# Optimization experiments

Measured on AMD Instinct MI355X. Metric: run time of the kernel, lower is better.

## Reference

```python
import jax, jax.numpy as jnp
import numpy as np

RANKS_HIGH = 15   # dt.RANKS.HIGH in the repo
SUITS_HIGH = 14   # padded so conv output last dim == 10 (Linear(10,32))
EPS = 1e-5


def _bn(x, g, b, axes):
    # Batch-norm over `axes` with channel dim = 1, training-mode batch stats.
    m = jnp.mean(x, axis=axes, keepdims=True)
    v = jnp.var(x, axis=axes, keepdims=True)
    xn = (x - m) * jax.lax.rsqrt(v + EPS)
    shp = [1] * x.ndim
    shp[1] = -1
    return xn * g.reshape(shp) + b.reshape(shp)


def setup_inputs() -> dict:
    key = jax.random.key(0)
    ks = jax.random.split(key, 16)
    M = 4096
    s = 0.05
    return {
        "x": jax.random.randint(ks[0], (M, 5, 2), 0, 4),  # (rank, suit) indices
        "conv_w": jax.random.normal(ks[1], (64, 5, 5, 5), jnp.float32) * s,
        "conv_b": jax.random.normal(ks[2], (64,), jnp.float32) * s,
        "bn0_g": jnp.ones((64,), jnp.float32),
        "bn0_b": jnp.zeros((64,), jnp.float32),
        "w_rank": jax.random.normal(ks[3], (32, 10), jnp.float32) * s,
        "b_rank": jax.random.normal(ks[4], (32,), jnp.float32) * s,
        "w_h1": jax.random.normal(ks[5], (32, 32), jnp.float32) * s,
        "b_h1": jax.random.normal(ks[6], (32,), jnp.float32) * s,
        "bn1_g": jnp.ones((64,), jnp.float32),
        "bn1_b": jnp.zeros((64,), jnp.float32),
        "w_h2": jax.random.normal(ks[7], (16, 32), jnp.float32) * s,
        "b_h2": jax.random.normal(ks[8], (16,), jnp.float32) * s,
        "bn2_g": jnp.ones((64,), jnp.float32),
        "bn2_b": jnp.zeros((64,), jnp.float32),
        "w_out": jax.random.normal(ks[9], (9, 11264), jnp.float32) * s,
        "b_out": jax.random.normal(ks[10], (9,), jnp.float32) * s,
    }


def reference(x, conv_w, conv_b, bn0_g, bn0_b, w_rank, b_rank, w_h1, b_h1,
              bn1_g, bn1_b, w_h2, b_h2, bn2_g, bn2_b, w_out, b_out):
    ranks = x[:, :, 0]
    suits = x[:, :, 1]
    # Vectorized replacement of the double Python-loop one-hot scatter:
    # three_d[j, i, ranks[j, i], suits[j, i]] = 1  ->  outer product of one-hots.
    three_d = (jax.nn.one_hot(ranks, RANKS_HIGH, dtype=jnp.float32)[..., :, None]
               * jax.nn.one_hot(suits, SUITS_HIGH, dtype=jnp.float32)[..., None, :])  # [M,5,15,14]
    r = jax.lax.conv_general_dilated(
        three_d, conv_w, window_strides=(1, 1), padding="VALID",
        dimension_numbers=("NCHW", "OIHW", "NCHW"))  # [M,64,11,10]
    r = r + conv_b[None, :, None, None]
    r = jax.nn.relu(_bn(r, bn0_g, bn0_b, (0, 2, 3)))
    r = jax.nn.relu(jnp.einsum("mchs,os->mcho", r, w_rank) + b_rank)      # [M,64,11,32]
    r = jnp.einsum("mchi,oi->mcho", r, w_h1) + b_h1                        # [M,64,11,32]
    r = jax.nn.relu(_bn(r, bn1_g, bn1_b, (0, 2, 3)))
    r = jnp.einsum("mchi,oi->mcho", r, w_h2) + b_h2                        # [M,64,11,16]
    r = jax.nn.relu(_bn(r, bn2_g, bn2_b, (0, 2, 3)))
    r = r.reshape(r.shape[0], -1)                                          # [M,11264]
    return r @ w_out.T + b_out                                             # [M,9]
```

## Files before the change

kernel.cpp:

```cpp
#include <hip/hip_runtime.h>
#include <hip/hip_bf16.h>

#define EPSV 1e-5f

typedef float vf2 __attribute__((ext_vector_type(2)));
typedef _Float16 h4f __attribute__((ext_vector_type(4)));

__device__ __forceinline__ vf2 pk_fma(vf2 a, vf2 b, vf2 c) {
  vf2 d;
  asm("v_pk_fma_f32 %0, %1, %2, %3" : "=v"(d) : "v"(a), "v"(b), "v"(c));
  return d;
}
__device__ __forceinline__ vf2 pk_mul(vf2 a, vf2 b) {
  vf2 d;
  asm("v_pk_mul_f32 %0, %1, %2" : "=v"(d) : "v"(a), "v"(b));
  return d;
}

#define WS_SUM0   0
#define WS_SSQ0   64
#define WS_SUM1   128
#define WS_SSQ1   192
#define WS_SUM2   256
#define WS_SSQ2   320
#define WS_AL0    384
#define WS_BE0    448
#define WS_ZBG    512
#define WS_T1BG   576
#define WS_AL1    2624
#define WS_BE1    2688
#define WS_T2BG   2752
#define WS_AL2    3776
#define WS_BE2    3840
#define WS_A2BG   3904
#define WS_OC     4928
#define WS_CU     4992
#define WS_CW     5120
#define WS_HIST   10304
#define WS_WSUM   13056
#define WS_T1     24576

#define CONV_LDS 5184
#define NHIST 2640

__device__ __forceinline__ void stage_conv(float* sW, const float* __restrict__ conv_w,
                                           int nthr) {
  for (int i = threadIdx.x; i < 8000; i += nthr) {
    int k = i / 125, rem = i - k * 125;
    int cc = rem / 25, r2 = rem - cc * 25;
    int di = r2 / 5, dj = r2 - di * 5;
    if (di < 4 && dj < 4) sW[k * 81 + cc * 16 + di * 4 + dj] = conv_w[i];
  }
  for (int k = threadIdx.x; k < 64; k += nthr) sW[k * 81 + 80] = 0.f;
}

__device__ __forceinline__ void stage_conv_fast(float* sW, const float* __restrict__ cw) {
  const float4* src = (const float4*)cw;
  float4* dst = (float4*)sW;
  for (int i = threadIdx.x; i < CONV_LDS / 4; i += 256) dst[i] = src[i];
}

__device__ __forceinline__ int conv_idx(int di, int dj, int cc) {
  int idx = cc * 16 + di * 4 + dj;
  return ((di | dj) >= 0) ? idx : 80;
}

__global__ __launch_bounds__(256) void k_prep3(
    const int* __restrict__ x, const float* __restrict__ conv_w,
    const float* __restrict__ w_out, float* __restrict__ ws, int M) {
  __shared__ float h[NHIST];
  const int b = blockIdx.x;
  const int tid = threadIdx.x;
  if (b < 8) {
    float* cw = ws + WS_CW;
    const int gid = b * 256 + tid;
    for (int i = gid; i < 8000; i += 8 * 256) {
      int k = i / 125, rem = i - k * 125;
      int cc = rem / 25, r2 = rem - cc * 25;
      int di = r2 / 5, dj = r2 - di * 5;
      if (di < 4 && dj < 4) cw[k * 81 + cc * 16 + di * 4 + dj] = conv_w[i];
    }
    for (int k = gid; k < 64; k += 8 * 256) cw[k * 81 + 80] = 0.f;
  } else if (b < 44) {
    const int gid = (b - 8) * 256 + tid;
    if (gid < 9216) {
      int j = gid / 1024, kp = gid - j * 1024;
      int k = kp >> 4, p = kp & 15;
      float s = 0.f;
#pragma unroll
      for (int yy = 4; yy < 11; ++yy)
        s += w_out[j * 11264 + k * 176 + yy * 16 + p];
      ws[WS_WSUM + gid] = s;
    }
  } else {
    for (int i = tid; i < NHIST; i += 256) h[i] = 0.f;
    __syncthreads();
    for (int m = (b - 44) * 256 + tid; m < M; m += 16 * 256) {
      int v[5];
      const int2* xp = (const int2*)(x + m * 10);
#pragma unroll
      for (int cc = 0; cc < 5; ++cc) {
        int2 t = xp[cc];
        v[cc] = (t.x << 2) | t.y;
      }
#pragma unroll
      for (int cc = 0; cc < 5; ++cc) atomicAdd(&h[cc * 16 + v[cc]], 1.f);
      int pr = 0;
#pragma unroll
      for (int a = 0; a < 5; ++a)
#pragma unroll
        for (int bb = a + 1; bb < 5; ++bb) {
          atomicAdd(&h[80 + pr * 256 + v[a] * 16 + v[bb]], 1.f);
          ++pr;
        }
    }
    __syncthreads();
    for (int i = tid; i < NHIST; i += 256)
      if (h[i] != 0.f) atomicAdd(&ws[WS_HIST + i], h[i]);
  }
}

__global__ __launch_bounds__(256) void k_stats0h(
    const float* __restrict__ conv_b, float* __restrict__ ws, int M) {
  __shared__ float sWk[81];
  __shared__ float sH[NHIST];
  const int tid = threadIdx.x;
  const int k = blockIdx.x;
  if (tid < 81) sWk[tid] = ws[WS_CW + k * 81 + tid];
  for (int i = tid; i < NHIST; i += 256) sH[i] = ws[WS_HIST + i];
  __syncthreads();
  const float cb = conv_b[k];
  float L = 0.f, Q = 0.f, P = 0.f;
  for (int it = tid; it < 1280; it += 256) {
    int pos = it / 80, rem = it - pos * 80;
    int cc = rem >> 4, v = rem & 15;
    int y = pos >> 2, xx = pos & 3;
    float w = sWk[conv_idx((v >> 2) - y, (v & 3) - xx, cc)];
    float n = sH[cc * 16 + v];
    L += n * w;
    Q += n * w * w;
  }
  if (tid < 160) {
    int pos = tid / 10, pr = tid - pos * 10;
    int y = pos >> 2, xx = pos & 3;
    int a, b;
    if (pr < 4)      { a = 0; b = pr + 1; }
    else if (pr < 7) { a = 1; b = pr - 2; }
    else if (pr < 9) { a = 2; b = pr - 4; }
    else             { a = 3; b = 4; }
    const float* Hp = sH + 80 + pr * 256;
    for (int v1 = 0; v1 < 16; ++v1) {
      float w1 = sWk[conv_idx((v1 >> 2) - y, (v1 & 3) - xx, a)];
      float acc = 0.f;
#pragma unroll
      for (int v2 = 0; v2 < 16; ++v2) {
        float w2 = sWk[conv_idx((v2 >> 2) - y, (v2 & 3) - xx, b)];
        acc += Hp[v1 * 16 + v2] * w2;
      }
      P += w1 * acc;
    }
  }
  atomicAdd(&ws[WS_SUM0 + k], L);
  atomicAdd(&ws[WS_SSQ0 + k], Q + 2.f * cb * L + 2.f * P);
  if (tid == 0) {
    const float a16 = 16.f * (float)M;
    atomicAdd(&ws[WS_SUM0 + k], a16 * cb);
    atomicAdd(&ws[WS_SSQ0 + k], a16 * cb * cb);
  }
}

__global__ __launch_bounds__(256) void k_t1(
    const int* __restrict__ x, const float* __restrict__ conv_b,
    const float* __restrict__ g0, const float* __restrict__ b0,
    const float* __restrict__ w_rank, const float* __restrict__ b_rank,
    const float* __restrict__ w_h1, const float* __restrict__ b_h1,
    float* __restrict__ ws, float* __restrict__ t1, int M) {
  __shared__ float sW[CONV_LDS];
  __shared__ float sCU[32];
  stage_conv_fast(sW, ws + WS_CW);
  if (threadIdx.x < 32) {
    float cuv = 0.f;
    for (int s2 = 4; s2 < 10; ++s2) cuv += w_rank[threadIdx.x * 10 + s2];
    sCU[threadIdx.x] = cuv;
  }
  __syncthreads();
  const int tid = threadIdx.x;
  const int y = tid & 3, k = tid >> 2;
  const float cb = conv_b[k];
  const float n0 = 110.f * (float)M;
  const float S0  = ws[WS_SUM0 + k] + 94.f * (float)M * cb;
  const float SS0 = ws[WS_SSQ0 + k] + 94.f * (float)M * cb * cb;
  const float mu0 = S0 / n0;
  const float var0 = SS0 / n0 - mu0 * mu0;
  const float al = rsqrtf(var0 + EPSV) * g0[k];
  const float be = b0[k] - mu0 * al;
  const float zbg = fmaxf(cb * al + be, 0.f);
  const float* Wk = &sW[k * 81];
  const vf2* wrp = (const vf2*)w_rank;
  const vf2* w1p = (const vf2*)w_h1;
  h4f* t1h = (h4f*)t1;
  float sAcc = 0.f, ssAcc = 0.f;
  const int NP = (M + 1) >> 1;
  for (int mp = blockIdx.x; mp < NP; mp += gridDim.x) {
    const int mA = mp * 2, mB = mA + 1;
    const bool hasB = (mB < M);
    const int mBs = hasB ? mB : mA;
    int rA[5], cA[5], rB[5], cBx[5];
    const int2* xpA = (const int2*)(x + mA * 10);
    const int2* xpB = (const int2*)(x + mBs * 10);
#pragma unroll
    for (int cc = 0; cc < 5; ++cc) {
      int2 tA = xpA[cc]; rA[cc] = tA.x; cA[cc] = tA.y;
      int2 tB = xpB[cc]; rB[cc] = tB.x; cBx[cc] = tB.y;
    }
    float a0A[4], a0B[4];
#pragma unroll
    for (int xx = 0; xx < 4; ++xx) {
      float vA = cb, vB = cb;
#pragma unroll
      for (int cc = 0; cc < 5; ++cc) {
        vA += Wk[conv_idx(rA[cc] - y, cA[cc] - xx, cc)];
        vB += Wk[conv_idx(rB[cc] - y, cBx[cc] - xx, cc)];
      }
      a0A[xx] = fmaxf(al * vA + be, 0.f);
      a0B[xx] = fmaxf(al * vB + be, 0.f);
    }
    vf2 aAp[2], aBp[2];
    aAp[0].x = a0A[0]; aAp[0].y = a0A[1];
    aAp[1].x = a0A[2]; aAp[1].y = a0A[3];
    aBp[0].x = a0B[0]; aBp[0].y = a0B[1];
    aBp[1].x = a0B[2]; aBp[1].y = a0B[3];
    __builtin_amdgcn_sched_barrier(0);
    vf2 r1A[16], r1B[16];
#pragma unroll
    for (int o2 = 0; o2 < 16; ++o2) {
      const int oa = 2 * o2, ob = oa + 1;
      vf2 w0 = wrp[oa * 5], w1 = wrp[oa * 5 + 1];
      vf2 w2 = wrp[ob * 5], w3 = wrp[ob * 5 + 1];
      const float basea = b_rank[oa] + zbg * sCU[oa];
      const float baseb = b_rank[ob] + zbg * sCU[ob];
      vf2 accAa = pk_mul(aAp[0], w0); accAa = pk_fma(aAp[1], w1, accAa);
      vf2 accAb = pk_mul(aAp[0], w2); accAb = pk_fma(aAp[1], w3, accAb);
      vf2 accBa = pk_mul(aBp[0], w0); accBa = pk_fma(aBp[1], w1, accBa);
      vf2 accBb = pk_mul(aBp[0], w2); accBb = pk_fma(aBp[1], w3, accBb);
      vf2 ra, rb;
      ra.x = fmaxf(basea + accAa.x + accAa.y, 0.f);
      ra.y = fmaxf(baseb + accAb.x + accAb.y, 0.f);
      rb.x = fmaxf(basea + accBa.x + accBa.y, 0.f);
      rb.y = fmaxf(baseb + accBb.x + accBb.y, 0.f);
      r1A[o2] = ra;
      r1B[o2] = rb;
    }
    __builtin_amdgcn_sched_barrier(0);
    float sBm = 0.f, ssBm = 0.f;
#pragma unroll
    for (int chv = 0; chv < 8; ++chv) {
      float accA[4], accB[4];
#pragma unroll
      for (int u = 0; u < 4; ++u) {
        const int o = chv * 4 + u;
        vf2 a2A = {0.f, 0.f}, a2B = {0.f, 0.f};
#pragma unroll
        for (int i = 0; i < 16; ++i) {
          vf2 w = w1p[o * 16 + i];
          a2A = pk_fma(r1A[i], w, a2A);
          a2B = pk_fma(r1B[i], w, a2B);
        }
        const float bb = b_h1[o];
        float aA = bb + a2A.x + a2A.y;
        float aB = bb + a2B.x + a2B.y;
        accA[u] = aA; accB[u] = aB;
        sAcc += aA; ssAcc += aA * aA;
        sBm += aB;  ssBm += aB * aB;
      }
      h4f stA;
      stA[0] = (_Float16)accA[0]; stA[1] = (_Float16)accA[1];
      stA[2] = (_Float16)accA[2]; stA[3] = (_Float16)accA[3];
      t1h[((size_t)mA * 8 + chv) * 256 + tid] = stA;
      if (hasB) {
        h4f stB;
        stB[0] = (_Float16)accB[0]; stB[1] = (_Float16)accB[1];
        stB[2] = (_Float16)accB[2]; stB[3] = (_Float16)accB[3];
        t1h[((size_t)mB * 8 + chv) * 256 + tid] = stB;
      }
      __builtin_amdgcn_sched_barrier(0);
    }
    if (hasB) { sAcc += sBm; ssAcc += ssBm; }
  }
  sAcc  += __shfl_xor(sAcc, 1);  sAcc  += __shfl_xor(sAcc, 2);
  ssAcc += __shfl_xor(ssAcc, 1); ssAcc += __shfl_xor(ssAcc, 2);
  if (y == 0) {
    atomicAdd(&ws[WS_SUM1 + k], sAcc);
    atomicAdd(&ws[WS_SSQ1 + k], ssAcc);
  }
}

__global__ __launch_bounds__(256) void k_mid(
    const float* __restrict__ conv_b, const float* __restrict__ g0,
    const float* __restrict__ b0, const float* __restrict__ w_rank,
    const float* __restrict__ b_rank, const float* __restrict__ w_h1,
    const float* __restrict__ b_h1, const float* __restrict__ g1,
    const float* __restrict__ b1, const float* __restrict__ w_h2,
    const float* __restrict__ b_h2, float* __restrict__ ws, int M) {
  __shared__ float sWr[320];
  __shared__ float sWh1[32 * 33];
  __shared__ float sWh2[16 * 33];
  __shared__ float sS[32], sZ[64];
  __shared__ float sR1[64 * 33];
  __shared__ float sT1b[64 * 33];
  const int tid = threadIdx.x;
  for (int i = tid; i < 320; i += 256) sWr[i] = w_rank[i];
  for (int i = tid; i < 1024; i += 256) sWh1[(i >> 5) * 33 + (i & 31)] = w_h1[i];
  for (int i = tid; i < 512; i += 256) sWh2[(i >> 5) * 33 + (i & 31)] = w_h2[i];
  if (tid < 64) {
    const float cb = conv_b[tid];
    const float n0 = 110.f * (float)M;
    const float S0  = ws[WS_SUM0 + tid] + 94.f * (float)M * cb;
    const float SS0 = ws[WS_SSQ0 + tid] + 94.f * (float)M * cb * cb;
    const float mu0 = S0 / n0;
    const float var0 = SS0 / n0 - mu0 * mu0;
    const float al = rsqrtf(var0 + EPSV) * g0[tid];
    const float be = b0[tid] - mu0 * al;
    sZ[tid] = fmaxf(cb * al + be, 0.f);
  }
  __syncthreads();
  if (tid < 32) {
    float s = 0.f;
    for (int s2 = 0; s2 < 10; ++s2) s += sWr[tid * 10 + s2];
    sS[tid] = s;
  }
  __syncthreads();
  const int k = tid >> 2, q = tid & 3;
  const float zbg = sZ[k];
#pragma unroll
  for (int u = 0; u < 8; ++u) {
    const int o = q * 8 + u;
    sR1[k * 33 + o] = fmaxf(zbg * sS[o] + b_rank[o], 0.f);
  }
  __syncthreads();
  float sb = 0.f, ssb = 0.f;
#pragma unroll
  for (int u = 0; u < 8; ++u) {
    const int o = q * 8 + u;
    float acc = b_h1[o];
#pragma unroll
    for (int i = 0; i < 32; ++i) acc += sR1[k * 33 + i] * sWh1[o * 33 + i];
    sT1b[k * 33 + o] = acc;
    sb += acc;
    ssb += acc * acc;
  }
  sb  += __shfl_xor(sb, 1);  sb  += __shfl_xor(sb, 2);
  ssb += __shfl_xor(ssb, 1); ssb += __shfl_xor(ssb, 2);
  const float n1 = (float)M * 11.f * 32.f;
  const float S1  = ws[WS_SUM1 + k] + 7.f * (float)M * sb;
  const float SS1 = ws[WS_SSQ1 + k] + 7.f * (float)M * ssb;
  const float mu1 = S1 / n1;
  const float var1 = SS1 / n1 - mu1 * mu1;
  const float al1 = rsqrtf(var1 + EPSV) * g1[k];
  const float be1 = b1[k] - mu1 * al1;
  if (q == 0) {
    ws[WS_AL1 + k] = al1;
    ws[WS_BE1 + k] = be1;
  }
  __syncthreads();
#pragma unroll
  for (int u = 0; u < 8; ++u) {
    const int o = q * 8 + u;
    sR1[k * 33 + o] = fmaxf(al1 * sT1b[k * 33 + o] + be1, 0.f);
  }
  __syncthreads();
  float sb2 = 0.f, ssb2 = 0.f;
#pragma unroll
  for (int v = 0; v < 4; ++v) {
    const int p = q * 4 + v;
    float acc = b_h2[p];
#pragma unroll
    for (int o = 0; o < 32; ++o) acc += sR1[k * 33 + o] * sWh2[p * 33 + o];
    ws[WS_T2BG + k * 16 + p] = acc;
    sb2 += acc;
    ssb2 += acc * acc;
  }
  sb2  += __shfl_xor(sb2, 1);  sb2  += __shfl_xor(sb2, 2);
  ssb2 += __shfl_xor(ssb2, 1); ssb2 += __shfl_xor(ssb2, 2);
  if (q == 0) {
    ws[WS_SUM2 + k] = 7.f * (float)M * sb2;
    ws[WS_SSQ2 + k] = 7.f * (float)M * ssb2;
  }
}

__global__ __launch_bounds__(256) void k_t2(
    const float* __restrict__ w_h2, const float* __restrict__ b_h2,
    float* __restrict__ ws, float* __restrict__ t1, int M) {
  const int tid = threadIdx.x;
  const int y = tid & 3, k = tid >> 2;
  const float al1 = ws[WS_AL1 + k], be1 = ws[WS_BE1 + k];
  const vf2* w2p = (const vf2*)w_h2;
  h4f* t1h = (h4f*)t1;
  float sAcc = 0.f, ssAcc = 0.f;
  const int NP = (M + 1) >> 1;
  for (int mp = blockIdx.x; mp < NP; mp += gridDim.x) {
    const int mA = mp * 2, mB = mA + 1;
    const bool hasB = (mB < M);
    const int mBs = hasB ? mB : mA;
    vf2 a1A[16], a1B[16];
#pragma unroll
    for (int chv = 0; chv < 8; ++chv) {
      h4f vA = t1h[((size_t)mA * 8 + chv) * 256 + tid];
      h4f vB = t1h[((size_t)mBs * 8 + chv) * 256 + tid];
      vf2 pA0, pA1, pB0, pB1;
      pA0.x = fmaxf(al1 * (float)vA[0] + be1, 0.f);
      pA0.y = fmaxf(al1 * (float)vA[1] + be1, 0.f);
      pA1.x = fmaxf(al1 * (float)vA[2] + be1, 0.f);
      pA1.y = fmaxf(al1 * (float)vA[3] + be1, 0.f);
      pB0.x = fmaxf(al1 * (float)vB[0] + be1, 0.f);
      pB0.y = fmaxf(al1 * (float)vB[1] + be1, 0.f);
      pB1.x = fmaxf(al1 * (float)vB[2] + be1, 0.f);
      pB1.y = fmaxf(al1 * (float)vB[3] + be1, 0.f);
      a1A[chv * 2] = pA0; a1A[chv * 2 + 1] = pA1;
      a1B[chv * 2] = pB0; a1B[chv * 2 + 1] = pB1;
    }
    __builtin_amdgcn_sched_barrier(0);
    float sBm = 0.f, ssBm = 0.f;
#pragma unroll
    for (int pv = 0; pv < 4; ++pv) {
      float accA[4], accB[4];
#pragma unroll
      for (int u = 0; u < 4; ++u) {
        const int p = pv * 4 + u;
        vf2 a2A = {0.f, 0.f}, a2B = {0.f, 0.f};
#pragma unroll
        for (int i = 0; i < 16; ++i) {
          vf2 w = w2p[p * 16 + i];
          a2A = pk_fma(a1A[i], w, a2A);
          a2B = pk_fma(a1B[i], w, a2B);
        }
        const float bb = b_h2[p];
        float aA = bb + a2A.x + a2A.y;
        float aB = bb + a2B.x + a2B.y;
        accA[u] = aA; accB[u] = aB;
        sAcc += aA; ssAcc += aA * aA;
        sBm += aB;  ssBm += aB * aB;
      }
      h4f stA;
      stA[0] = (_Float16)accA[0]; stA[1] = (_Float16)accA[1];
      stA[2] = (_Float16)accA[2]; stA[3] = (_Float16)accA[3];
      t1h[((size_t)mA * 8 + pv) * 256 + tid] = stA;
      if (hasB) {
        h4f stB;
        stB[0] = (_Float16)accB[0]; stB[1] = (_Float16)accB[1];
        stB[2] = (_Float16)accB[2]; stB[3] = (_Float16)accB[3];
        t1h[((size_t)mB * 8 + pv) * 256 + tid] = stB;
      }
      __builtin_amdgcn_sched_barrier(0);
    }
    if (hasB) { sAcc += sBm; ssAcc += ssBm; }
  }
  sAcc  += __shfl_xor(sAcc, 1);  sAcc  += __shfl_xor(sAcc, 2);
  ssAcc += __shfl_xor(ssAcc, 1); ssAcc += __shfl_xor(ssAcc, 2);
  if (y == 0) {
    atomicAdd(&ws[WS_SUM2 + k], sAcc);
    atomicAdd(&ws[WS_SSQ2 + k], ssAcc);
  }
}

__global__ __launch_bounds__(256) void k_fin2p(
    const float* __restrict__ g2, const float* __restrict__ b2,
    const float* __restrict__ b_out, float* __restrict__ ws, int M) {
  __shared__ float sT2b[1024];
  __shared__ float sWs[9216];
  __shared__ float sAl2[64], sBe2[64];
  __shared__ float red[64 * 9];
  const int tid = threadIdx.x;
  for (int i = tid; i < 1024; i += 256) sT2b[i] = ws[WS_T2BG + i];
  for (int i = tid; i < 9216; i += 256) sWs[i] = ws[WS_WSUM + i];
  if (tid < 64) {
    const int k = tid;
    const float n2 = (float)M * 11.f * 16.f;
    const float S = ws[WS_SUM2 + k], SS = ws[WS_SSQ2 + k];
    const float mu = S / n2;
    const float var = SS / n2 - mu * mu;
    const float al = rsqrtf(var + EPSV) * g2[k];
    const float be = b2[k] - mu * al;
    sAl2[k] = al; sBe2[k] = be;
    ws[WS_AL2 + k] = al;
    ws[WS_BE2 + k] = be;
  }
  __syncthreads();
  for (int u = tid; u < 576; u += 256) {
    const int k = u / 9, j = u - k * 9;
    const float al = sAl2[k], be = sBe2[k];
    float acc = 0.f;
#pragma unroll
    for (int p = 0; p < 16; ++p)
      acc += fmaxf(al * sT2b[k * 16 + p] + be, 0.f) * sWs[j * 1024 + k * 16 + p];
    red[k * 9 + j] = acc;
  }
  __syncthreads();
  if (tid < 9) {
    float acc = b_out[tid];
    for (int t = 0; t < 64; ++t) acc += red[t * 9 + tid];
    ws[WS_OC + tid] = acc;
  }
}

__global__ __launch_bounds__(256) void k_out(
    const float* __restrict__ w_out, const float* __restrict__ ws,
    const float* __restrict__ t1, float* __restrict__ out, int M) {
  __shared__ float sOC[9];
  __shared__ float sRedA[4][9], sRedB[4][9];
  if (threadIdx.x < 9) sOC[threadIdx.x] = ws[WS_OC + threadIdx.x];
  __syncthreads();
  const int tid = threadIdx.x;
  const int lane = tid & 63, wv = tid >> 6;
  const int y = tid & 3, k = tid >> 2;
  const float al2 = ws[WS_AL2 + k], be2 = ws[WS_BE2 + k];
  const float4* wo = (const float4*)(w_out + k * 176 + y * 16);
  const h4f* t2h = (const h4f*)t1;
  const int NP = (M + 1) >> 1;
  bool first = true;
  for (int mp = blockIdx.x; mp < NP; mp += gridDim.x) {
    if (!first) __syncthreads();
    first = false;
    const int mA = mp * 2, mB = mA + 1;
    const bool hasB = (mB < M);
    const int mBs = hasB ? mB : mA;
    vf2 a2A[8], a2B[8];
#pragma unroll
    for (int iv = 0; iv < 4; ++iv) {
      h4f vA = t2h[((size_t)mA * 8 + iv) * 256 + tid];
      h4f vB = t2h[((size_t)mBs * 8 + iv) * 256 + tid];
      vf2 pA0, pA1, pB0, pB1;
      pA0.x = fmaxf(al2 * (float)vA[0] + be2, 0.f);
      pA0.y = fmaxf(al2 * (float)vA[1] + be2, 0.f);
      pA1.x = fmaxf(al2 * (float)vA[2] + be2, 0.f);
      pA1.y = fmaxf(al2 * (float)vA[3] + be2, 0.f);
      pB0.x = fmaxf(al2 * (float)vB[0] + be2, 0.f);
      pB0.y = fmaxf(al2 * (float)vB[1] + be2, 0.f);
      pB1.x = fmaxf(al2 * (float)vB[2] + be2, 0.f);
      pB1.y = fmaxf(al2 * (float)vB[3] + be2, 0.f);
      a2A[iv * 2] = pA0; a2A[iv * 2 + 1] = pA1;
      a2B[iv * 2] = pB0; a2B[iv * 2 + 1] = pB1;
    }
    float poA[9], poB[9];
#pragma unroll
    for (int j = 0; j < 9; ++j) {
      float4 w0 = wo[j * 2816 + 0], w1 = wo[j * 2816 + 1];
      float4 w2 = wo[j * 2816 + 2], w3 = wo[j * 2816 + 3];
      vf2 aA = {0.f, 0.f}, aB = {0.f, 0.f};
      vf2 t;
      t.x = w0.x; t.y = w0.y; aA = pk_fma(a2A[0], t, aA); aB = pk_fma(a2B[0], t, aB);
      t.x = w0.z; t.y = w0.w; aA = pk_fma(a2A[1], t, aA); aB = pk_fma(a2B[1], t, aB);
      t.x = w1.x; t.y = w1.y; aA = pk_fma(a2A[2], t, aA); aB = pk_fma(a2B[2], t, aB);
      t.x = w1.z; t.y = w1.w; aA = pk_fma(a2A[3], t, aA); aB = pk_fma(a2B[3], t, aB);
      t.x = w2.x; t.y = w2.y; aA = pk_fma(a2A[4], t, aA); aB = pk_fma(a2B[4], t, aB);
      t.x = w2.z; t.y = w2.w; aA = pk_fma(a2A[5], t, aA); aB = pk_fma(a2B[5], t, aB);
      t.x = w3.x; t.y = w3.y; aA = pk_fma(a2A[6], t, aA); aB = pk_fma(a2B[6], t, aB);
      t.x = w3.z; t.y = w3.w; aA = pk_fma(a2A[7], t, aA); aB = pk_fma(a2B[7], t, aB);
      poA[j] = aA.x + aA.y;
      poB[j] = aB.x + aB.y;
    }
#pragma unroll
    for (int j = 0; j < 9; ++j) {
      float vA = poA[j], vB = poB[j];
      vA += __shfl_xor(vA, 1);  vB += __shfl_xor(vB, 1);
      vA += __shfl_xor(vA, 2);  vB += __shfl_xor(vB, 2);
      vA += __shfl_xor(vA, 4);  vB += __shfl_xor(vB, 4);
      vA += __shfl_xor(vA, 8);  vB += __shfl_xor(vB, 8);
      vA += __shfl_xor(vA, 16); vB += __shfl_xor(vB, 16);
      vA += __shfl_xor(vA, 32); vB += __shfl_xor(vB, 32);
      poA[j] = vA; poB[j] = vB;
    }
    if (lane == 0) {
#pragma unroll
      for (int j = 0; j < 9; ++j) { sRedA[wv][j] = poA[j]; sRedB[wv][j] = poB[j]; }
    }
    __syncthreads();
    if (tid < 9) {
      float acc = sOC[tid];
#pragma unroll
      for (int w2i = 0; w2i < 4; ++w2i) acc += sRedA[w2i][tid];
      out[mA * 9 + tid] = acc;
    } else if (tid >= 64 && tid < 73 && hasB) {
      const int j = tid - 64;
      float acc = sOC[j];
#pragma unroll
      for (int w2i = 0; w2i < 4; ++w2i) acc += sRedB[w2i][j];
      out[mB * 9 + j] = acc;
    }
  }
}

__global__ __launch_bounds__(64) void k_fin0(
    const float* __restrict__ conv_b, const float* __restrict__ g0,
    const float* __restrict__ b0, const float* __restrict__ w_rank,
    const float* __restrict__ b_rank, const float* __restrict__ w_h1,
    const float* __restrict__ b_h1, float* __restrict__ ws, int M) {
  __shared__ float sS[32];
  const int t = threadIdx.x;
  if (t < 32) {
    float su = 0.f;
    for (int s2 = 0; s2 < 10; ++s2) su += w_rank[t * 10 + s2];
    sS[t] = su;
    float cu = 0.f;
    for (int s2 = 4; s2 < 10; ++s2) cu += w_rank[t * 10 + s2];
    ws[WS_CU + t] = cu;
  }
  __syncthreads();
  const int k = t;
  const float n0 = 110.f * (float)M;
  const float cb = conv_b[k];
  const float S  = ws[WS_SUM0 + k] + 94.f * (float)M * cb;
  const float SS = ws[WS_SSQ0 + k] + 94.f * (float)M * cb * cb;
  const float mu = S / n0;
  const float var = SS / n0 - mu * mu;
  const float rstd = rsqrtf(var + EPSV);
  const float al = rstd * g0[k];
  const float be = b0[k] - mu * al;
  ws[WS_AL0 + k] = al;
  ws[WS_BE0 + k] = be;
  const float zbg = fmaxf(cb * al + be, 0.f);
  ws[WS_ZBG + k] = zbg;
  float r1bg[32];
#pragma unroll
  for (int o = 0; o < 32; ++o) r1bg[o] = fmaxf(zbg * sS[o] + b_rank[o], 0.f);
  float sb = 0.f, ssb = 0.f;
  for (int o = 0; o < 32; ++o) {
    float acc = b_h1[o];
#pragma unroll
    for (int i = 0; i < 32; ++i) acc += r1bg[i] * w_h1[o * 32 + i];
    ws[WS_T1BG + k * 32 + o] = acc;
    sb += acc;
    ssb += acc * acc;
  }
  ws[WS_SUM1 + k] = 7.f * (float)M * sb;
  ws[WS_SSQ1 + k] = 7.f * (float)M * ssb;
}

__global__ __launch_bounds__(64) void k_fin1(
    const float* __restrict__ g1, const float* __restrict__ b1,
    const float* __restrict__ w_h2, const float* __restrict__ b_h2,
    float* __restrict__ ws, int M) {
  const int k = threadIdx.x;
  const float n1 = (float)M * 11.f * 32.f;
  const float S = ws[WS_SUM1 + k], SS = ws[WS_SSQ1 + k];
  const float mu = S / n1;
  const float var = SS / n1 - mu * mu;
  const float rstd = rsqrtf(var + EPSV);
  const float al = rstd * g1[k];
  const float be = b1[k] - mu * al;
  ws[WS_AL1 + k] = al;
  ws[WS_BE1 + k] = be;
  float a1bg[32];
#pragma unroll
  for (int o = 0; o < 32; ++o)
    a1bg[o] = fmaxf(al * ws[WS_T1BG + k * 32 + o] + be, 0.f);
  float sb = 0.f, ssb = 0.f;
  for (int p = 0; p < 16; ++p) {
    float acc = b_h2[p];
#pragma unroll
    for (int o = 0; o < 32; ++o) acc += a1bg[o] * w_h2[p * 32 + o];
    ws[WS_T2BG + k * 16 + p] = acc;
    sb += acc;
    ssb += acc * acc;
  }
  ws[WS_SUM2 + k] = 7.f * (float)M * sb;
  ws[WS_SSQ2 + k] = 7.f * (float)M * ssb;
}

__global__ __launch_bounds__(256) void k_stats0(
    const int* __restrict__ x, const float* __restrict__ conv_w,
    const float* __restrict__ conv_b, float* __restrict__ ws, int M) {
  __shared__ float sW[CONV_LDS];
  stage_conv(sW, conv_w, 256);
  __syncthreads();
  const int tid = threadIdx.x;
  const int mg = tid & 3;
  const int k  = tid >> 2;
  const float cb = conv_b[k];
  const float* Wk = &sW[k * 81];
  float s = 0.f, ss = 0.f;
  for (int m = blockIdx.x * 4 + mg; m < M; m += gridDim.x * 4) {
    int r[5], c[5];
    const int2* xp = (const int2*)(x + m * 10);
#pragma unroll
    for (int cc = 0; cc < 5; ++cc) { int2 t = xp[cc]; r[cc] = t.x; c[cc] = t.y; }
#pragma unroll
    for (int y = 0; y < 4; ++y) {
#pragma unroll
      for (int xx = 0; xx < 4; ++xx) {
        float v = cb;
#pragma unroll
        for (int cc = 0; cc < 5; ++cc)
          v += Wk[conv_idx(r[cc] - y, c[cc] - xx, cc)];
        s += v;
        ss += v * v;
      }
      __builtin_amdgcn_sched_barrier(0);
    }
  }
  s  += __shfl_xor(s, 1);  s  += __shfl_xor(s, 2);
  ss += __shfl_xor(ss, 1); ss += __shfl_xor(ss, 2);
  if (mg == 0) {
    atomicAdd(&ws[WS_SUM0 + k], s);
    atomicAdd(&ws[WS_SSQ0 + k], ss);
  }
}

__global__ __launch_bounds__(256) void k_stats1(
    const int* __restrict__ x, const float* __restrict__ conv_w,
    const float* __restrict__ conv_b, const float* __restrict__ w_rank,
    const float* __restrict__ b_rank, const float* __restrict__ w_h1,
    const float* __restrict__ b_h1, float* __restrict__ ws, int M) {
  __shared__ float sW[CONV_LDS];
  stage_conv(sW, conv_w, 256);
  __syncthreads();
  const int tid = threadIdx.x;
  const int y = tid & 3, k = tid >> 2;
  const float cb = conv_b[k];
  const float al = ws[WS_AL0 + k], be = ws[WS_BE0 + k], zbg = ws[WS_ZBG + k];
  const float* Wk = &sW[k * 81];
  const float* cu = ws + WS_CU;
  float sAcc = 0.f, ssAcc = 0.f;
  for (int m = blockIdx.x; m < M; m += gridDim.x) {
    int r[5], c[5];
    const int2* xp = (const int2*)(x + m * 10);
#pragma unroll
    for (int cc = 0; cc < 5; ++cc) { int2 t = xp[cc]; r[cc] = t.x; c[cc] = t.y; }
    float a0[4];
#pragma unroll
    for (int xx = 0; xx < 4; ++xx) {
      float v = cb;
#pragma unroll
      for (int cc = 0; cc < 5; ++cc)
        v += Wk[conv_idx(r[cc] - y, c[cc] - xx, cc)];
      a0[xx] = fmaxf(al * v + be, 0.f);
    }
    __builtin_amdgcn_sched_barrier(0);
    float r1[32];
#pragma unroll
    for (int o = 0; o < 32; ++o) {
// ... 135 lines not shown
      for (int yy = 4; yy < 11; ++yy)
        wsum += w_out[j * 11264 + k * 176 + yy * 16 + p];
      acc += a2bg[p] * wsum;
    }
    red[k * 9 + j] = acc;
  }
  __syncthreads();
  if (k < 9) {
    float acc = b_out[k];
    for (int t = 0; t < 64; ++t) acc += red[t * 9 + k];
    ws[WS_OC + k] = acc;
  }
}

__global__ __launch_bounds__(256) void k_final(
    const int* __restrict__ x, const float* __restrict__ conv_w,
    const float* __restrict__ conv_b, const float* __restrict__ w_rank,
    const float* __restrict__ b_rank, const float* __restrict__ w_h1,
    const float* __restrict__ b_h1, const float* __restrict__ w_h2,
    const float* __restrict__ b_h2, const float* __restrict__ w_out,
    const float* __restrict__ ws, float* __restrict__ out, int M) {
  __shared__ float sW[CONV_LDS];
  __shared__ float sOC[9];
  __shared__ float sRed[4][9];
  stage_conv(sW, conv_w, 256);
  if (threadIdx.x < 9) sOC[threadIdx.x] = ws[WS_OC + threadIdx.x];
  __syncthreads();
  const int tid = threadIdx.x;
  const int lane = tid & 63, wv = tid >> 6;
  const int y = tid & 3, k = tid >> 2;
  const float cb = conv_b[k];
  const float al = ws[WS_AL0 + k], be = ws[WS_BE0 + k], zbg = ws[WS_ZBG + k];
  const float al1 = ws[WS_AL1 + k], be1 = ws[WS_BE1 + k];
  const float al2 = ws[WS_AL2 + k], be2 = ws[WS_BE2 + k];
  const float* Wk = &sW[k * 81];
  const float* cu = ws + WS_CU;
  const float4* wo = (const float4*)(w_out + k * 176 + y * 16);
  bool first = true;
  for (int m = blockIdx.x; m < M; m += gridDim.x) {
    if (!first) __syncthreads();
    first = false;
    int r[5], c[5];
    const int2* xp = (const int2*)(x + m * 10);
#pragma unroll
    for (int cc = 0; cc < 5; ++cc) { int2 t = xp[cc]; r[cc] = t.x; c[cc] = t.y; }
    float a0[4];
#pragma unroll
    for (int xx = 0; xx < 4; ++xx) {
      float v = cb;
#pragma unroll
      for (int cc = 0; cc < 5; ++cc)
        v += Wk[conv_idx(r[cc] - y, c[cc] - xx, cc)];
      a0[xx] = fmaxf(al * v + be, 0.f);
    }
    __builtin_amdgcn_sched_barrier(0);
    float r1[32];
#pragma unroll
    for (int o = 0; o < 32; ++o) {
      float acc = b_rank[o] + zbg * cu[o];
#pragma unroll
      for (int xx = 0; xx < 4; ++xx) acc += a0[xx] * w_rank[o * 10 + xx];
      r1[o] = fmaxf(acc, 0.f);
    }
    __builtin_amdgcn_sched_barrier(0);
    float t2[16];
#pragma unroll
    for (int p = 0; p < 16; ++p) t2[p] = b_h2[p];
#pragma unroll
    for (int ch = 0; ch < 4; ++ch) {
      float a1c[8];
#pragma unroll
      for (int u = 0; u < 8; ++u) {
        const int o = ch * 8 + u;
        float acc = b_h1[o];
#pragma unroll
        for (int i = 0; i < 32; ++i) acc += r1[i] * w_h1[o * 32 + i];
        a1c[u] = fmaxf(al1 * acc + be1, 0.f);
      }
      __builtin_amdgcn_sched_barrier(0);
#pragma unroll
      for (int p = 0; p < 16; ++p) {
        float acc = t2[p];
#pragma unroll
        for (int u = 0; u < 8; ++u) acc += a1c[u] * w_h2[p * 32 + ch * 8 + u];
        t2[p] = acc;
      }
      __builtin_amdgcn_sched_barrier(0);
    }
    float a2[16];
#pragma unroll
    for (int p = 0; p < 16; ++p) a2[p] = fmaxf(al2 * t2[p] + be2, 0.f);
    float po[9];
#pragma unroll
    for (int j = 0; j < 9; ++j) {
      float4 w0 = wo[j * 2816 + 0], w1 = wo[j * 2816 + 1];
      float4 w2 = wo[j * 2816 + 2], w3 = wo[j * 2816 + 3];
      po[j] = a2[0] * w0.x + a2[1] * w0.y + a2[2] * w0.z + a2[3] * w0.w
            + a2[4] * w1.x + a2[5] * w1.y + a2[6] * w1.z + a2[7] * w1.w
            + a2[8] * w2.x + a2[9] * w2.y + a2[10] * w2.z + a2[11] * w2.w
            + a2[12] * w3.x + a2[13] * w3.y + a2[14] * w3.z + a2[15] * w3.w;
    }
#pragma unroll
    for (int j = 0; j < 9; ++j) {
      float v = po[j];
      v += __shfl_xor(v, 1);
      v += __shfl_xor(v, 2);
      v += __shfl_xor(v, 4);
      v += __shfl_xor(v, 8);
      v += __shfl_xor(v, 16);
      v += __shfl_xor(v, 32);
      po[j] = v;
    }
    if (lane == 0) {
#pragma unroll
      for (int j = 0; j < 9; ++j) sRed[wv][j] = po[j];
    }
    __syncthreads();
    if (tid < 9) {
      float acc = sOC[tid];
#pragma unroll
      for (int w2i = 0; w2i < 4; ++w2i) acc += sRed[w2i][tid];
      out[m * 9 + tid] = acc;
    }
  }
}

extern "C" void kernel_launch(void* const* d_in, const int* in_sizes, int n_in,
                              void* d_out, int out_size, void* d_ws, size_t ws_size,
                              hipStream_t stream) {
  const int*   x      = (const int*)d_in[0];
  const float* conv_w = (const float*)d_in[1];
  const float* conv_b = (const float*)d_in[2];
  const float* bn0_g  = (const float*)d_in[3];
  const float* bn0_b  = (const float*)d_in[4];
  const float* w_rank = (const float*)d_in[5];
  const float* b_rank = (const float*)d_in[6];
  const float* w_h1   = (const float*)d_in[7];
  const float* b_h1   = (const float*)d_in[8];
  const float* bn1_g  = (const float*)d_in[9];
  const float* bn1_b  = (const float*)d_in[10];
  const float* w_h2   = (const float*)d_in[11];
  const float* b_h2   = (const float*)d_in[12];
  const float* bn2_g  = (const float*)d_in[13];
  const float* bn2_b  = (const float*)d_in[14];
  const float* w_out  = (const float*)d_in[15];
  const float* b_out  = (const float*)d_in[16];
  float* out = (float*)d_out;
  float* ws  = (float*)d_ws;
  const int M = in_sizes[0] / 10;
  const size_t need = ((size_t)WS_T1 + (size_t)M * 4096) * sizeof(float);
  const int NP = (M + 1) >> 1;
  const int gridp = NP < 2048 ? NP : 2048;

  hipMemsetAsync(ws, 0, 384 * sizeof(float), stream);

  if (ws_size >= need) {
    float* t1 = ws + WS_T1;
    hipMemsetAsync(ws + WS_HIST, 0, NHIST * sizeof(float), stream);
    k_prep3<<<60, 256, 0, stream>>>(x, conv_w, w_out, ws, M);
    k_stats0h<<<64, 256, 0, stream>>>(conv_b, ws, M);
    k_t1<<<gridp, 256, 0, stream>>>(x, conv_b, bn0_g, bn0_b, w_rank, b_rank,
                                    w_h1, b_h1, ws, t1, M);
    k_mid<<<1, 256, 0, stream>>>(conv_b, bn0_g, bn0_b, w_rank, b_rank, w_h1, b_h1,
                                 bn1_g, bn1_b, w_h2, b_h2, ws, M);
    k_t2<<<gridp, 256, 0, stream>>>(w_h2, b_h2, ws, t1, M);
    k_fin2p<<<1, 256, 0, stream>>>(bn2_g, bn2_b, b_out, ws, M);
    k_out<<<gridp, 256, 0, stream>>>(w_out, ws, t1, out, M);
  } else {
    k_stats0<<<512, 256, 0, stream>>>(x, conv_w, conv_b, ws, M);
    k_fin0<<<1, 64, 0, stream>>>(conv_b, bn0_g, bn0_b, w_rank, b_rank, w_h1, b_h1, ws, M);
    k_stats1<<<1024, 256, 0, stream>>>(x, conv_w, conv_b, w_rank, b_rank, w_h1, b_h1,
                                       ws, M);
    k_fin1<<<1, 64, 0, stream>>>(bn1_g, bn1_b, w_h2, b_h2, ws, M);
    k_stats2<<<1024, 256, 0, stream>>>(x, conv_w, conv_b, w_rank, b_rank, w_h1, b_h1,
                                       w_h2, b_h2, ws, M);
    k_fin2<<<1, 64, 0, stream>>>(bn2_g, bn2_b, w_out, b_out, ws, M);
    k_final<<<1024, 256, 0, stream>>>(x, conv_w, conv_b, w_rank, b_rank, w_h1, b_h1,
                                      w_h2, b_h2, w_out, ws, out, M);
  }
}
```

Before: 303.2 us.

## Drop memsets and k_mid launch; per-slice histograms and fold mid-stats into consumers

Removes the two hipMemsetAsync calls by writing per-slice histograms and having k_stats0h write, rather than atomically add, the stats and zero the later accumulators. The single-block k_mid kernel is removed: its BN0/BN1 background computations are recomputed redundantly in every k_t2 block and in k_fin2p, which now also derives the BN2 background stats. k_out replaces its shuffle-based output reduction with an LDS transpose and a two-level sum. Together these cut kernel launches and serialized tiny kernels, at the cost of redundant per-block recomputation and more LDS use.

```diff
diff --git a/kernel.cpp b/kernel.cpp
--- a/kernel.cpp
+++ b/kernel.cpp
@@ -36,9 +36,9 @@
 #define WS_OC     4928
 #define WS_CU     4992
 #define WS_CW     5120
-#define WS_HIST   10304
-#define WS_WSUM   13056
-#define WS_T1     24576
+#define WS_WSUM   10304
+#define WS_HSL    19584
+#define WS_T1     65536
 
 #define CONV_LDS 5184
 #define NHIST 2640
@@ -93,9 +93,10 @@
       ws[WS_WSUM + gid] = s;
     }
   } else {
+    const int slice = b - 44;
     for (int i = tid; i < NHIST; i += 256) h[i] = 0.f;
     __syncthreads();
-    for (int m = (b - 44) * 256 + tid; m < M; m += 16 * 256) {
+    for (int m = slice * 256 + tid; m < M; m += 16 * 256) {
       int v[5];
       const int2* xp = (const int2*)(x + m * 10);
 #pragma unroll
@@ -116,7 +117,7 @@
     }
     __syncthreads();
     for (int i = tid; i < NHIST; i += 256)
-      if (h[i] != 0.f) atomicAdd(&ws[WS_HIST + i], h[i]);
+      ws[WS_HSL + slice * NHIST + i] = h[i];
   }
 }
 
@@ -124,10 +125,16 @@
     const float* __restrict__ conv_b, float* __restrict__ ws, int M) {
   __shared__ float sWk[81];
   __shared__ float sH[NHIST];
+  __shared__ float sRed[8];
   const int tid = threadIdx.x;
   const int k = blockIdx.x;
   if (tid < 81) sWk[tid] = ws[WS_CW + k * 81 + tid];
-  for (int i = tid; i < NHIST; i += 256) sH[i] = ws[WS_HIST + i];
+  for (int i = tid; i < NHIST; i += 256) {
+    float s = 0.f;
+#pragma unroll
+    for (int sl = 0; sl < 16; ++sl) s += ws[WS_HSL + sl * NHIST + i];
+    sH[i] = s;
+  }
   __syncthreads();
   const float cb = conv_b[k];
   float L = 0.f, Q = 0.f, P = 0.f;
@@ -160,12 +167,26 @@
       P += w1 * acc;
     }
   }
-  atomicAdd(&ws[WS_SUM0 + k], L);
-  atomicAdd(&ws[WS_SSQ0 + k], Q + 2.f * cb * L + 2.f * P);
+  float A = L, B = Q + 2.f * cb * L + 2.f * P;
+  A += __shfl_xor(A, 1);  B += __shfl_xor(B, 1);
+  A += __shfl_xor(A, 2);  B += __shfl_xor(B, 2);
+  A += __shfl_xor(A, 4);  B += __shfl_xor(B, 4);
+  A += __shfl_xor(A, 8);  B += __shfl_xor(B, 8);
+  A += __shfl_xor(A, 16); B += __shfl_xor(B, 16);
+  A += __shfl_xor(A, 32); B += __shfl_xor(B, 32);
+  const int lane = tid & 63, wv = tid >> 6;
+  if (lane == 0) { sRed[wv * 2] = A; sRed[wv * 2 + 1] = B; }
+  __syncthreads();
   if (tid == 0) {
+    float At = sRed[0] + sRed[2] + sRed[4] + sRed[6];
+    float Bt = sRed[1] + sRed[3] + sRed[5] + sRed[7];
     const float a16 = 16.f * (float)M;
-    atomicAdd(&ws[WS_SUM0 + k], a16 * cb);
-    atomicAdd(&ws[WS_SSQ0 + k], a16 * cb * cb);
+    ws[WS_SUM0 + k] = At + a16 * cb;
+    ws[WS_SSQ0 + k] = Bt + a16 * cb * cb;
+    ws[WS_SUM1 + k] = 0.f;
+    ws[WS_SSQ1 + k] = 0.f;
+    ws[WS_SUM2 + k] = 0.f;
+    ws[WS_SSQ2 + k] = 0.f;
   }
 }
 
@@ -295,105 +316,55 @@
   }
 }
 
-__global__ __launch_bounds__(256) void k_mid(
+__global__ __launch_bounds__(256) void k_t2(
     const float* __restrict__ conv_b, const float* __restrict__ g0,
     const float* __restrict__ b0, const float* __restrict__ w_rank,
     const float* __restrict__ b_rank, const float* __restrict__ w_h1,
     const float* __restrict__ b_h1, const float* __restrict__ g1,
     const float* __restrict__ b1, const float* __restrict__ w_h2,
-    const float* __restrict__ b_h2, float* __restrict__ ws, int M) {
-  __shared__ float sWr[320];
-  __shared__ float sWh1[32 * 33];
-  __shared__ float sWh2[16 * 33];
-  __shared__ float sS[32], sZ[64];
-  __shared__ float sR1[64 * 33];
-  __shared__ float sT1b[64 * 33];
+    const float* __restrict__ b_h2, float* __restrict__ ws,
+    float* __restrict__ t1, int M) {
+  __shared__ float sS[32];
+  __shared__ float sWh1[1024];
   const int tid = threadIdx.x;
-  for (int i = tid; i < 320; i += 256) sWr[i] = w_rank[i];
-  for (int i = tid; i < 1024; i += 256) sWh1[(i >> 5) * 33 + (i & 31)] = w_h1[i];
-  for (int i = tid; i < 512; i += 256) sWh2[(i >> 5) * 33 + (i & 31)] = w_h2[i];
-  if (tid < 64) {
-    const float cb = conv_b[tid];
-    const float n0 = 110.f * (float)M;
-    const float S0  = ws[WS_SUM0 + tid] + 94.f * (float)M * cb;
-    const float SS0 = ws[WS_SSQ0 + tid] + 94.f * (float)M * cb * cb;
-    const float mu0 = S0 / n0;
-    const float var0 = SS0 / n0 - mu0 * mu0;
-    const float al = rsqrtf(var0 + EPSV) * g0[tid];
-    const float be = b0[tid] - mu0 * al;
-    sZ[tid] = fmaxf(cb * al + be, 0.f);
-  }
-  __syncthreads();
+  for (int i = tid; i < 1024; i += 256) sWh1[i] = w_h1[i];
   if (tid < 32) {
     float s = 0.f;
-    for (int s2 = 0; s2 < 10; ++s2) s += sWr[tid * 10 + s2];
+    for (int s2 = 0; s2 < 10; ++s2) s += w_rank[tid * 10 + s2];
     sS[tid] = s;
   }
   __syncthreads();
-  const int k = tid >> 2, q = tid & 3;
-  const float zbg = sZ[k];
+  const int y = tid & 3, k = tid >> 2;
+  const float fM = (float)M;
+  const float cb = conv_b[k];
+  const float n0 = 110.f * fM;
+  const float S0  = ws[WS_SUM0 + k] + 94.f * fM * cb;
+  const float SS0 = ws[WS_SSQ0 + k] + 94.f * fM * cb * cb;
+  const float mu0 = S0 / n0;
+  const float al0 = rsqrtf(SS0 / n0 - mu0 * mu0 + EPSV) * g0[k];
+  const float be0 = b0[k] - mu0 * al0;
+  const float zbg = fmaxf(cb * al0 + be0, 0.f);
+  float r1bg[32];
+#pragma unroll
+  for (int o = 0; o < 32; ++o) r1bg[o] = fmaxf(zbg * sS[o] + b_rank[o], 0.f);
+  float sb = 0.f, ssb = 0.f;
 #pragma unroll
   for (int u = 0; u < 8; ++u) {
-    const int o = q * 8 + u;
-    sR1[k * 33 + o] = fmaxf(zbg * sS[o] + b_rank[o], 0.f);
-  }
-  __syncthreads();
-  float sb = 0.f, ssb = 0.f;
-#pragma unroll
-  for (int u = 0; u < 8; ++u) {
-    const int o = q * 8 + u;
-    float acc = b_h1[o];
-#pragma unroll
-    for (int i = 0; i < 32; ++i) acc += sR1[k * 33 + i] * sWh1[o * 33 + i];
-    sT1b[k * 33 + o] = acc;
-    sb += acc;
-    ssb += acc * acc;
+    const int o = y * 8 + u;
+    float a = b_h1[o];
+#pragma unroll
+    for (int i = 0; i < 32; ++i) a += r1bg[i] * sWh1[o * 32 + i];
+    sb += a;
+    ssb += a * a;
   }
   sb  += __shfl_xor(sb, 1);  sb  += __shfl_xor(sb, 2);
   ssb += __shfl_xor(ssb, 1); ssb += __shfl_xor(ssb, 2);
-  const float n1 = (float)M * 11.f * 32.f;
-  const float S1  = ws[WS_SUM1 + k] + 7.f * (float)M * sb;
-  const float SS1 = ws[WS_SSQ1 + k] + 7.f * (float)M * ssb;
+  const float n1 = fM * 11.f * 32.f;
+  const float S1  = ws[WS_SUM1 + k] + 7.f * fM * sb;
+  const float SS1 = ws[WS_SSQ1 + k] + 7.f * fM * ssb;
   const float mu1 = S1 / n1;
-  const float var1 = SS1 / n1 - mu1 * mu1;
-  const float al1 = rsqrtf(var1 + EPSV) * g1[k];
+  const float al1 = rsqrtf(SS1 / n1 - mu1 * mu1 + EPSV) * g1[k];
   const float be1 = b1[k] - mu1 * al1;
-  if (q == 0) {
-    ws[WS_AL1 + k] = al1;
-    ws[WS_BE1 + k] = be1;
-  }
-  __syncthreads();
-#pragma unroll
-  for (int u = 0; u < 8; ++u) {
-    const int o = q * 8 + u;
-    sR1[k * 33 + o] = fmaxf(al1 * sT1b[k * 33 + o] + be1, 0.f);
-  }
-  __syncthreads();
-  float sb2 = 0.f, ssb2 = 0.f;
-#pragma unroll
-  for (int v = 0; v < 4; ++v) {
-    const int p = q * 4 + v;
-    float acc = b_h2[p];
-#pragma unroll
-    for (int o = 0; o < 32; ++o) acc += sR1[k * 33 + o] * sWh2[p * 33 + o];
-    ws[WS_T2BG + k * 16 + p] = acc;
-    sb2 += acc;
-    ssb2 += acc * acc;
-  }
-  sb2  += __shfl_xor(sb2, 1);  sb2  += __shfl_xor(sb2, 2);
-  ssb2 += __shfl_xor(ssb2, 1); ssb2 += __shfl_xor(ssb2, 2);
-  if (q == 0) {
-    ws[WS_SUM2 + k] = 7.f * (float)M * sb2;
-    ws[WS_SSQ2 + k] = 7.f * (float)M * ssb2;
-  }
-}
-
-__global__ __launch_bounds__(256) void k_t2(
-    const float* __restrict__ w_h2, const float* __restrict__ b_h2,
-    float* __restrict__ ws, float* __restrict__ t1, int M) {
-  const int tid = threadIdx.x;
-  const int y = tid & 3, k = tid >> 2;
-  const float al1 = ws[WS_AL1 + k], be1 = ws[WS_BE1 + k];
   const vf2* w2p = (const vf2*)w_h2;
   h4f* t1h = (h4f*)t1;
   float sAcc = 0.f, ssAcc = 0.f;
@@ -464,36 +435,110 @@
 }
 
 __global__ __launch_bounds__(256) void k_fin2p(
-    const float* __restrict__ g2, const float* __restrict__ b2,
-    const float* __restrict__ b_out, float* __restrict__ ws, int M) {
-  __shared__ float sT2b[1024];
+    const float* __restrict__ conv_b, const float* __restrict__ g0,
+    const float* __restrict__ b0, const float* __restrict__ w_rank,
+    const float* __restrict__ b_rank, const float* __restrict__ w_h1,
+    const float* __restrict__ b_h1, const float* __restrict__ g1,
+    const float* __restrict__ b1, const float* __restrict__ w_h2,
+    const float* __restrict__ b_h2, const float* __restrict__ g2,
+    const float* __restrict__ b2, const float* __restrict__ b_out,
+    float* __restrict__ ws, int M) {
+  __shared__ float sS[32];
+  __shared__ float sWh1[1024];
+  __shared__ float sWh2[512];
   __shared__ float sWs[9216];
-  __shared__ float sAl2[64], sBe2[64];
-  __shared__ float red[64 * 9];
+  __shared__ float sA2[1024];
+  __shared__ float red[576];
   const int tid = threadIdx.x;
-  for (int i = tid; i < 1024; i += 256) sT2b[i] = ws[WS_T2BG + i];
+  for (int i = tid; i < 1024; i += 256) sWh1[i] = w_h1[i];
+  for (int i = tid; i < 512; i += 256) sWh2[i] = w_h2[i];
   for (int i = tid; i < 9216; i += 256) sWs[i] = ws[WS_WSUM + i];
-  if (tid < 64) {
-    const int k = tid;
-    const float n2 = (float)M * 11.f * 16.f;
-    const float S = ws[WS_SUM2 + k], SS = ws[WS_SSQ2 + k];
-    const float mu = S / n2;
-    const float var = SS / n2 - mu * mu;
-    const float al = rsqrtf(var + EPSV) * g2[k];
-    const float be = b2[k] - mu * al;
-    sAl2[k] = al; sBe2[k] = be;
-    ws[WS_AL2 + k] = al;
-    ws[WS_BE2 + k] = be;
+  if (tid < 32) {
+    float s = 0.f;
+    for (int s2 = 0; s2 < 10; ++s2) s += w_rank[tid * 10 + s2];
+    sS[tid] = s;
+  }
+  __syncthreads();
+  const int k = tid >> 2, q = tid & 3;
+  const float fM = (float)M;
+  const float cb = conv_b[k];
+  const float n0 = 110.f * fM;
+  const float S0  = ws[WS_SUM0 + k] + 94.f * fM * cb;
+  const float SS0 = ws[WS_SSQ0 + k] + 94.f * fM * cb * cb;
+  const float mu0 = S0 / n0;
+  const float al0 = rsqrtf(SS0 / n0 - mu0 * mu0 + EPSV) * g0[k];
+  const float be0 = b0[k] - mu0 * al0;
+  const float zbg = fmaxf(cb * al0 + be0, 0.f);
+  float r1bg[32];
+#pragma unroll
+  for (int o = 0; o < 32; ++o) r1bg[o] = fmaxf(zbg * sS[o] + b_rank[o], 0.f);
+  float t1bg[8];
+  float sb = 0.f, ssb = 0.f;
+#pragma unroll
+  for (int u = 0; u < 8; ++u) {
+    const int o = q * 8 + u;
+    float a = b_h1[o];
+#pragma unroll
+    for (int i = 0; i < 32; ++i) a += r1bg[i] * sWh1[o * 32 + i];
+    t1bg[u] = a;
+    sb += a;
+    ssb += a * a;
+  }
+  sb  += __shfl_xor(sb, 1);  sb  += __shfl_xor(sb, 2);
+  ssb += __shfl_xor(ssb, 1); ssb += __shfl_xor(ssb, 2);
+  const float n1 = fM * 11.f * 32.f;
+  const float S1  = ws[WS_SUM1 + k] + 7.f * fM * sb;
+  const float SS1 = ws[WS_SSQ1 + k] + 7.f * fM * ssb;
+  const float mu1 = S1 / n1;
+  const float al1 = rsqrtf(SS1 / n1 - mu1 * mu1 + EPSV) * g1[k];
+  const float be1 = b1[k] - mu1 * al1;
+  float a1bg[8];
+#pragma unroll
+  for (int u = 0; u < 8; ++u) a1bg[u] = fmaxf(al1 * t1bg[u] + be1, 0.f);
+  float pt[16];
+#pragma unroll
+  for (int p = 0; p < 16; ++p) {
+    float a = 0.f;
+#pragma unroll
+    for (int u = 0; u < 8; ++u) a += a1bg[u] * sWh2[p * 32 + q * 8 + u];
+    pt[p] = a;
+  }
+#pragma unroll
+  for (int p = 0; p < 16; ++p) {
+    pt[p] += __shfl_xor(pt[p], 1);
+    pt[p] += __shfl_xor(pt[p], 2);
+  }
+  float sb2 = 0.f, ssb2 = 0.f;
+#pragma unroll
+  for (int p = 0; p < 16; ++p) {
+    float v = pt[p] + b_h2[p];
+    pt[p] = v;
+    sb2 += v;
+    ssb2 += v * v;
+  }
+  const float n2 = fM * 11.f * 16.f;
+  const float S2  = ws[WS_SUM2 + k] + 7.f * fM * sb2;
+  const float SS2 = ws[WS_SSQ2 + k] + 7.f * fM * ssb2;
+  const float mu2 = S2 / n2;
+  const float al2 = rsqrtf(SS2 / n2 - mu2 * mu2 + EPSV) * g2[k];
+  const float be2 = b2[k] - mu2 * al2;
+  if (q == 0) {
+    ws[WS_AL2 + k] = al2;
+    ws[WS_BE2 + k] = be2;
+  }
+#pragma unroll
+  for (int v2 = 0; v2 < 4; ++v2) {
+    const int p = q * 4 + v2;
+    sA2[k * 16 + p] = fmaxf(al2 * pt[p] + be2, 0.f);
   }
   __syncthreads();
   for (int u = tid; u < 576; u += 256) {
-    const int k = u / 9, j = u - k * 9;
-    const float al = sAl2[k], be = sBe2[k];
+    const int kk = u / 9, j = u - kk * 9;
     float acc = 0.f;
 #pragma unroll
     for (int p = 0; p < 16; ++p)
-      acc += fmaxf(al * sT2b[k * 16 + p] + be, 0.f) * sWs[j * 1024 + k * 16 + p];
-    red[k * 9 + j] = acc;
+      acc += sA2[kk * 16 + p] * sWs[j * 1024 + kk * 16 + p];
+    red[u] = acc;
   }
   __syncthreads();
   if (tid < 9) {
@@ -507,11 +552,10 @@
     const float* __restrict__ w_out, const float* __restrict__ ws,
     const float* __restrict__ t1, float* __restrict__ out, int M) {
   __shared__ float sOC[9];
-  __shared__ float sRedA[4][9], sRedB[4][9];
+  __shared__ float sP[256][19];
+  __shared__ float sR2[18 * 8];
   if (threadIdx.x < 9) sOC[threadIdx.x] = ws[WS_OC + threadIdx.x];
-  __syncthreads();
   const int tid = threadIdx.x;
-  const int lane = tid & 63, wv = tid >> 6;
   const int y = tid & 3, k = tid >> 2;
   const float al2 = ws[WS_AL2 + k], be2 = ws[WS_BE2 + k];
   const float4* wo = (const float4*)(w_out + k * 176 + y * 16);
@@ -541,7 +585,6 @@
       a2A[iv * 2] = pA0; a2A[iv * 2 + 1] = pA1;
       a2B[iv * 2] = pB0; a2B[iv * 2 + 1] = pB1;
     }
-    float poA[9], poB[9];
 #pragma unroll
     for (int j = 0; j < 9; ++j) {
       float4 w0 = wo[j * 2816 + 0], w1 = wo[j * 2816 + 1];
@@ -556,36 +599,24 @@
       t.x = w2.z; t.y = w2.w; aA = pk_fma(a2A[5], t, aA); aB = pk_fma(a2B[5], t, aB);
       t.x = w3.x; t.y = w3.y; aA = pk_fma(a2A[6], t, aA); aB = pk_fma(a2B[6], t, aB);
       t.x = w3.z; t.y = w3.w; aA = pk_fma(a2A[7], t, aA); aB = pk_fma(a2B[7], t, aB);
-      poA[j] = aA.x + aA.y;
-      poB[j] = aB.x + aB.y;
-    }
-#pragma unroll
-    for (int j = 0; j < 9; ++j) {
-      float vA = poA[j], vB = poB[j];
-      vA += __shfl_xor(vA, 1);  vB += __shfl_xor(vB, 1);
-      vA += __shfl_xor(vA, 2);  vB += __shfl_xor(vB, 2);
-      vA += __shfl_xor(vA, 4);  vB += __shfl_xor(vB, 4);
-      vA += __shfl_xor(vA, 8);  vB += __shfl_xor(vB, 8);
-      vA += __shfl_xor(vA, 16); vB += __shfl_xor(vB, 16);
-      vA += __shfl_xor(vA, 32); vB += __shfl_xor(vB, 32);
-      poA[j] = vA; poB[j] = vB;
-    }
-    if (lane == 0) {
-#pragma unroll
-      for (int j = 0; j < 9; ++j) { sRedA[wv][j] = poA[j]; sRedB[wv][j] = poB[j]; }
+      sP[tid][j] = aA.x + aA.y;
+      sP[tid][9 + j] = aB.x + aB.y;
     }
     __syncthreads();
-    if (tid < 9) {
-      float acc = sOC[tid];
-#pragma unroll
-      for (int w2i = 0; w2i < 4; ++w2i) acc += sRedA[w2i][tid];
-      out[mA * 9 + tid] = acc;
-    } else if (tid >= 64 && tid < 73 && hasB) {
-      const int j = tid - 64;
-      float acc = sOC[j];
-#pragma unroll
-      for (int w2i = 0; w2i < 4; ++w2i) acc += sRedB[w2i][j];
-      out[mB * 9 + j] = acc;
+    if (tid < 144) {
+      const int slot = tid / 8, part = tid & 7;
+      float s = 0.f;
+#pragma unroll 8
+      for (int t = 0; t < 32; ++t) s += sP[part + t * 8][slot];
+      sR2[slot * 8 + part] = s;
+    }
+    __syncthreads();
+    if (tid < 18) {
+      float s = 0.f;
+#pragma unroll
+      for (int p8 = 0; p8 < 8; ++p8) s += sR2[tid * 8 + p8];
+      if (tid < 9) out[mA * 9 + tid] = sOC[tid] + s;
+      else if (hasB) out[mB * 9 + (tid - 9)] = sOC[tid - 9] + s;
     }
   }
 }
@@ -1027,21 +1058,21 @@
   const int NP = (M + 1) >> 1;
   const int gridp = NP < 2048 ? NP : 2048;
 
-  hipMemsetAsync(ws, 0, 384 * sizeof(float), stream);
-
   if (ws_size >= need) {
     float* t1 = ws + WS_T1;
-    hipMemsetAsync(ws + WS_HIST, 0, NHIST * sizeof(float), stream);
     k_prep3<<<60, 256, 0, stream>>>(x, conv_w, w_out, ws, M);
     k_stats0h<<<64, 256, 0, stream>>>(conv_b, ws, M);
     k_t1<<<gridp, 256, 0, stream>>>(x, conv_b, bn0_g, bn0_b, w_rank, b_rank,
                                     w_h1, b_h1, ws, t1, M);
-    k_mid<<<1, 256, 0, stream>>>(conv_b, bn0_g, bn0_b, w_rank, b_rank, w_h1, b_h1,
-                                 bn1_g, bn1_b, w_h2, b_h2, ws, M);
-    k_t2<<<gridp, 256, 0, stream>>>(w_h2, b_h2, ws, t1, M);
-    k_fin2p<<<1, 256, 0, stream>>>(bn2_g, bn2_b, b_out, ws, M);
+    k_t2<<<gridp, 256, 0, stream>>>(conv_b, bn0_g, bn0_b, w_rank, b_rank,
+                                    w_h1, b_h1, bn1_g, bn1_b, w_h2, b_h2,
+                                    ws, t1, M);
+    k_fin2p<<<1, 256, 0, stream>>>(conv_b, bn0_g, bn0_b, w_rank, b_rank,
+                                   w_h1, b_h1, bn1_g, bn1_b, w_h2, b_h2,
+                                   bn2_g, bn2_b, b_out, ws, M);
     k_out<<<gridp, 256, 0, stream>>>(w_out, ws, t1, out, M);
   } else {
+    hipMemsetAsync(ws, 0, 384 * sizeof(float), stream);
     k_stats0<<<512, 256, 0, stream>>>(x, conv_w, conv_b, ws, M);
     k_fin0<<<1, 64, 0, stream>>>(conv_b, bn0_g, bn0_b, w_rank, b_rank, w_h1, b_h1, ws, M);
     k_stats1<<<1024, 256, 0, stream>>>(x, conv_w, conv_b, w_rank, b_rank, w_h1, b_h1,
```

After: 301.5 us. Within noise of the previous version (-0.6%).
